# Optimization experiments

Measured on AMD Instinct MI355X. Metric: run time of the kernel, lower is better.

## Reference

```python
import jax, jax.numpy as jnp
import numpy as np

B, S, D_IN, D_OUT = 4, 2048, 1024, 1024


def setup_inputs() -> dict:
    key = jax.random.key(0)
    kx, kq, kk, kv = jax.random.split(key, 4)
    scale = 1.0 / np.sqrt(D_IN)
    return {
        "x": jax.random.normal(kx, (B, S, D_IN), dtype=jnp.float32),
        "W_q": jax.random.normal(kq, (D_IN, D_OUT), dtype=jnp.float32) * scale,
        "W_k": jax.random.normal(kk, (D_IN, D_OUT), dtype=jnp.float32) * scale,
        "W_v": jax.random.normal(kv, (D_IN, D_OUT), dtype=jnp.float32) * scale,
    }


def reference(x, W_q, W_k, W_v):
    # QKV projections (Linear without bias): [B,S,D_out]
    q = jnp.einsum("bsd,de->bse", x, W_q)
    k = jnp.einsum("bsd,de->bse", x, W_k)
    v = jnp.einsum("bsd,de->bse", x, W_v)

    # Raw scores [B,S,S], causal mask (strict upper triangle -> -inf),
    # then scale by sqrt(d_k) and softmax, matching the torch order of ops.
    scores = jnp.einsum("bqd,bkd->bqk", q, k)
    seq = scores.shape[-1]
    causal = jnp.triu(jnp.ones((seq, seq), dtype=bool), k=1)
    scores = jnp.where(causal[None, :, :], -jnp.inf, scores)
    attn = jax.nn.softmax(scores / jnp.sqrt(jnp.asarray(q.shape[-1], scores.dtype)), axis=-1)
    # dropout p=0.0 -> identity (eval semantics)
    return jnp.einsum("bqk,bkd->bqd", attn, v)
```

## Files before the change

### kernel.cpp

```cpp
#include <hip/hip_runtime.h>

typedef unsigned short u16;
typedef __bf16 bf16x8 __attribute__((ext_vector_type(8)));
typedef float f32x4 __attribute__((ext_vector_type(4)));

__device__ __forceinline__ u16 f2bf(float f) {
    union { float f; unsigned int u; } v; v.f = f;
    unsigned int u = v.u;
    return (u16)((u + 0x7FFFu + ((u >> 16) & 1u)) >> 16);
}

__device__ __forceinline__ void load_lds16(const void* g, void* l) {
    __builtin_amdgcn_global_load_lds(
        (const __attribute__((address_space(1))) unsigned int*)g,
        (__attribute__((address_space(3))) unsigned int*)l,
        16, 0, 0);
}

__global__ void __launch_bounds__(256) prep_kernel(
    const float4* __restrict__ X, u16* __restrict__ xb,
    const float* __restrict__ Wq, const float* __restrict__ Wk,
    const float* __restrict__ Wv,
    u16* __restrict__ Oq, u16* __restrict__ Ok, u16* __restrict__ Ov,
    float* __restrict__ rowsum) {
    __shared__ float tile[32][33];
    const int bid = blockIdx.x, tid = threadIdx.x;
    if (bid < 8192) {
        int idx = bid * 256 + tid;
        float4 v = X[idx];
        ushort4 o;
        o.x = f2bf(v.x); o.y = f2bf(v.y); o.z = f2bf(v.z); o.w = f2bf(v.w);
        *(ushort4*)(xb + (size_t)idx * 4) = o;
    } else if (bid < 11264) {
        int id = bid - 8192;
        int zz = id >> 10;
        const float* W = (zz == 0) ? Wq : (zz == 1) ? Wk : Wv;
        u16* O = (zz == 0) ? Oq : (zz == 1) ? Ok : Ov;
        int n0 = (id & 31) * 32, k0 = ((id >> 5) & 31) * 32;
        int tx = tid & 31, ty = tid >> 5;
        #pragma unroll
        for (int j = 0; j < 32; j += 8)
            tile[ty + j][tx] = W[(size_t)(k0 + ty + j) * 1024 + n0 + tx];
        __syncthreads();
        #pragma unroll
        for (int j = 0; j < 32; j += 8)
            O[(size_t)(n0 + ty + j) * 1024 + k0 + tx] = f2bf(tile[tx][ty + j]);
    } else {
        rowsum[(bid - 11264) * 256 + tid] = 0.f;
    }
}

template <int MODE>
__global__ void __launch_bounds__(256) gemm_nt(
    const u16* __restrict__ xb, const u16* __restrict__ WqT,
    const u16* __restrict__ WkT, const u16* __restrict__ WvT,
    u16* __restrict__ Q, u16* __restrict__ Kb,
    u16* __restrict__ Vt, u16* __restrict__ S,
    float* __restrict__ rowsum, float* __restrict__ out) {

    int mtile, ntile, z;
    const u16 *A, *B;
    int vsub = 0;

    if (MODE == 0) {
        int L = blockIdx.x;
        int c = L & 7, t = (L >> 3) & 7, hi = L >> 6;
        int p = hi * 8 + c;
        z = p >> 6; mtile = p & 63; ntile = t;
        A = xb;
        B = z ? WkT : WqT;
    } else if (MODE == 1) {
        if (blockIdx.x < 512) {
            vsub = 1;
            int id = blockIdx.x;
            int c = id & 7, t = (id >> 3) & 7, hi = id >> 6;
            mtile = hi * 8 + c; ntile = t; z = 0;
            A = xb; B = WvT;
        } else {
            int id2 = blockIdx.x - 512;
            z = id2 / 192;
            int r = id2 - z * 192;
            int c = r & 7, g = r >> 3;
            if (g <= c)            { mtile = c;     ntile = g; }
            else if (g < 2*c + 10) { mtile = c + 8; ntile = g - (c + 1); }
            else return;
            A = Q  + (size_t)z * (2048 * 1024);
            B = Kb + (size_t)z * (2048 * 1024);
        }
    } else {
        int L = blockIdx.x;
        ntile = L & 7;
        int j = L >> 3;
        z = j & 3; mtile = 15 - (j >> 2);
        A = S  + (size_t)z * (2048 * 2048);
        B = Vt + (size_t)z * (1024 * 2048);
    }

    const int LDA = (MODE == 3) ? 2048 : 1024;
    const int kiters = (MODE == 3) ? (mtile + 1) * 2 : 16;

    __shared__ __align__(16) u16 As[2][128 * 32];
    __shared__ __align__(16) u16 Bs[2][128 * 32];

    const int tid = threadIdx.x;
    const int lane = tid & 63;
    const int wave = tid >> 6;
    const int wr = wave >> 1, wc = wave & 1;

    const int r0 = tid >> 2;
    const int kb = (((tid & 3) ^ ((r0 >> 1) & 3))) * 16;

    const char* gA0 = (const char*)(A + (size_t)(mtile * 128 + r0) * LDA) + kb;
    const char* gA1 = gA0 + (size_t)64 * LDA * 2;
    const char* gB0 = (const char*)(B + (size_t)(ntile * 128 + r0) * LDA) + kb;
    const char* gB1 = gB0 + (size_t)64 * LDA * 2;

    char* lA = (char*)(&As[0][0]) + tid * 16;
    char* lB = (char*)(&Bs[0][0]) + tid * 16;

    f32x4 acc[4][4] = {};

    const int quad = lane >> 4;
    const int l16 = lane & 15;
    const int ch = quad ^ ((l16 >> 1) & 3);
    const int aoff = (wr * 64 + l16) * 32 + ch * 8;
    const int boff = (wc * 64 + l16) * 32 + ch * 8;

    for (int kt = 0; kt < kiters; ++kt) {
        load_lds16(gA0,      lA);
        load_lds16(gA1,      lA + 4096);
        load_lds16(gA0 + 64, lA + 8192);
        load_lds16(gA1 + 64, lA + 12288);
        load_lds16(gB0,      lB);
        load_lds16(gB1,      lB + 4096);
        load_lds16(gB0 + 64, lB + 8192);
        load_lds16(gB1 + 64, lB + 12288);
        gA0 += 128; gA1 += 128; gB0 += 128; gB1 += 128;
        __syncthreads();

        #pragma unroll
        for (int h2 = 0; h2 < 2; ++h2) {
            const u16* ap = &As[h2][aoff];
            const u16* bp = &Bs[h2][boff];
            bf16x8 af[4], bfv[4];
            #pragma unroll
            for (int r = 0; r < 4; ++r) af[r] = *(const bf16x8*)(ap + r * 512);
            #pragma unroll
            for (int c = 0; c < 4; ++c) bfv[c] = *(const bf16x8*)(bp + c * 512);
            #pragma unroll
            for (int r = 0; r < 4; ++r)
                #pragma unroll
                for (int c = 0; c < 4; ++c)
                    acc[r][c] = __builtin_amdgcn_mfma_f32_16x16x32_bf16(
                        af[r], bfv[c], acc[r][c], 0, 0, 0);
        }
        __syncthreads();
    }

    const int grow0 = mtile * 128 + wr * 64 + quad * 4;
    const int gcol0 = ntile * 128 + wc * 64 + l16;

    if (MODE == 0) {
        u16* C = z ? Kb : Q;
        #pragma unroll
        for (int r = 0; r < 4; ++r)
            #pragma unroll
            for (int c = 0; c < 4; ++c)
                #pragma unroll
                for (int i = 0; i < 4; ++i)
                    C[(size_t)(grow0 + r * 16 + i) * 1024 + gcol0 + c * 16] =
                        f2bf(acc[r][c][i]);
    } else if (MODE == 1) {
        if (vsub) {
            #pragma unroll
            for (int r = 0; r < 4; ++r) {
                int m0 = grow0 + r * 16;
                int b = m0 >> 11, s0 = m0 & 2047;
                #pragma unroll
                for (int c = 0; c < 4; ++c) {
                    int d = gcol0 + c * 16;
                    ushort4 o;
                    o.x = f2bf(acc[r][c][0]); o.y = f2bf(acc[r][c][1]);
                    o.z = f2bf(acc[r][c][2]); o.w = f2bf(acc[r][c][3]);
                    *(ushort4*)(Vt + (size_t)b * (1024 * 2048) + (size_t)d * 2048 + s0) = o;
                }
            }
        } else {
            u16* C = S + (size_t)z * (2048 * 2048);
            float* rs = rowsum + z * 2048;
            const bool diag = (ntile == mtile);
            float rsum[4][4];
            #pragma unroll
            for (int r = 0; r < 4; ++r)
                #pragma unroll
                for (int i = 0; i < 4; ++i) rsum[r][i] = 0.f;
            #pragma unroll
            for (int r = 0; r < 4; ++r)
                #pragma unroll
                for (int c = 0; c < 4; ++c)
                    #pragma unroll
                    for (int i = 0; i < 4; ++i) {
                        int grow = grow0 + r * 16 + i;
                        int gcol = gcol0 + c * 16;
                        float e = 0.f;
                        if (!diag || gcol <= grow)
                            e = __expf(acc[r][c][i] * 0.03125f - 12.0f);
                        C[(size_t)grow * 2048 + gcol] = f2bf(e);
                        rsum[r][i] += e;
                    }
            #pragma unroll
            for (int r = 0; r < 4; ++r)
                #pragma unroll
                for (int i = 0; i < 4; ++i) {
                    float s = rsum[r][i];
                    s += __shfl_xor(s, 1, 64);
                    s += __shfl_xor(s, 2, 64);
                    s += __shfl_xor(s, 4, 64);
                    s += __shfl_xor(s, 8, 64);
                    if (l16 == 0)
                        atomicAdd(&rs[grow0 + r * 16 + i], s);
                }
        }
    } else {
        const float* rs = rowsum + z * 2048;
        float* C = out + (size_t)z * (2048 * 1024);
        #pragma unroll
        for (int r = 0; r < 4; ++r)
            #pragma unroll
            for (int i = 0; i < 4; ++i) {
                int grow = grow0 + r * 16 + i;
                float inv = 1.0f / rs[grow];
                #pragma unroll
                for (int c = 0; c < 4; ++c)
                    C[(size_t)grow * 1024 + gcol0 + c * 16] = acc[r][c][i] * inv;
            }
    }
}

extern "C" void kernel_launch(void* const* d_in, const int* in_sizes, int n_in,
                              void* d_out, int out_size, void* d_ws, size_t ws_size,
                              hipStream_t stream) {
    const float* x  = (const float*)d_in[0];
    const float* Wq = (const float*)d_in[1];
    const float* Wk = (const float*)d_in[2];
    const float* Wv = (const float*)d_in[3];
    float* out = (float*)d_out;
    char* ws = (char*)d_ws;
    const size_t Mi = 1u << 20;

    u16* xb  = (u16*)(ws);
    u16* WqT = (u16*)(ws + 16 * Mi);
    u16* WkT = (u16*)(ws + 18 * Mi);
    u16* WvT = (u16*)(ws + 20 * Mi);
    u16* Q   = (u16*)(ws + 22 * Mi);
    u16* Kb  = (u16*)(ws + 38 * Mi);
    u16* Vt  = (u16*)(ws + 54 * Mi);
    u16* S   = (u16*)(ws + 70 * Mi);
    float* rowsum = (float*)(ws + 102 * Mi);

    prep_kernel<<<11296, 256, 0, stream>>>(
        (const float4*)x, xb, Wq, Wk, Wv, WqT, WkT, WvT, rowsum);

    gemm_nt<0><<<1024, 256, 0, stream>>>(xb, WqT, WkT, WvT, Q, Kb, Vt, S, rowsum, out);

    gemm_nt<1><<<1280, 256, 0, stream>>>(xb, WqT, WkT, WvT, Q, Kb, Vt, S, rowsum, out);

    gemm_nt<3><<<512, 256, 0, stream>>>(xb, WqT, WkT, WvT, Q, Kb, Vt, S, rowsum, out);
}
```

Before: 236.3 us.

## Double-buffer LDS loads in GEMM and move V projection into QK launch

The GEMM main loop now uses the two LDS halves as ping-pong buffers with a 32-wide K step. The next tile's global-to-LDS loads are issued before computing on the current one, so memory latency overlaps MFMA work. The V projection moves from the scores launch into the Q/K projection launch (1536 blocks), leaving the scores launch with only the causal QK^T tiles. The mode index for the PV GEMM changes from 3 to 2. Each iteration does half the MFMA work per barrier pair, so synchronisation overhead per FLOP rises.

```diff
diff --git a/kernel.cpp b/kernel.cpp
--- a/kernel.cpp
+++ b/kernel.cpp
@@ -60,7 +60,6 @@
 
     int mtile, ntile, z;
     const u16 *A, *B;
-    int vsub = 0;
 
     if (MODE == 0) {
         int L = blockIdx.x;
@@ -68,25 +67,17 @@
         int p = hi * 8 + c;
         z = p >> 6; mtile = p & 63; ntile = t;
         A = xb;
-        B = z ? WkT : WqT;
+        B = (z == 0) ? WqT : (z == 1) ? WkT : WvT;
     } else if (MODE == 1) {
-        if (blockIdx.x < 512) {
-            vsub = 1;
-            int id = blockIdx.x;
-            int c = id & 7, t = (id >> 3) & 7, hi = id >> 6;
-            mtile = hi * 8 + c; ntile = t; z = 0;
-            A = xb; B = WvT;
-        } else {
-            int id2 = blockIdx.x - 512;
-            z = id2 / 192;
-            int r = id2 - z * 192;
-            int c = r & 7, g = r >> 3;
-            if (g <= c)            { mtile = c;     ntile = g; }
-            else if (g < 2*c + 10) { mtile = c + 8; ntile = g - (c + 1); }
-            else return;
-            A = Q  + (size_t)z * (2048 * 1024);
-            B = Kb + (size_t)z * (2048 * 1024);
-        }
+        int id2 = blockIdx.x;
+        z = id2 / 192;
+        int r = id2 - z * 192;
+        int c = r & 7, g = r >> 3;
+        if (g <= c)            { mtile = c;     ntile = g; }
+        else if (g < 2*c + 10) { mtile = c + 8; ntile = g - (c + 1); }
+        else return;
+        A = Q  + (size_t)z * (2048 * 1024);
+        B = Kb + (size_t)z * (2048 * 1024);
     } else {
         int L = blockIdx.x;
         ntile = L & 7;
@@ -96,8 +87,8 @@
         B = Vt + (size_t)z * (1024 * 2048);
     }
 
-    const int LDA = (MODE == 3) ? 2048 : 1024;
-    const int kiters = (MODE == 3) ? (mtile + 1) * 2 : 16;
+    const int LDA = (MODE == 2) ? 2048 : 1024;
+    const int kiters = (MODE == 2) ? (mtile + 1) * 4 : 32;
 
     __shared__ __align__(16) u16 As[2][128 * 32];
     __shared__ __align__(16) u16 Bs[2][128 * 32];
@@ -126,52 +117,58 @@
     const int aoff = (wr * 64 + l16) * 32 + ch * 8;
     const int boff = (wc * 64 + l16) * 32 + ch * 8;
 
-    for (int kt = 0; kt < kiters; ++kt) {
-        load_lds16(gA0,      lA);
-        load_lds16(gA1,      lA + 4096);
-        load_lds16(gA0 + 64, lA + 8192);
-        load_lds16(gA1 + 64, lA + 12288);
-        load_lds16(gB0,      lB);
-        load_lds16(gB1,      lB + 4096);
-        load_lds16(gB0 + 64, lB + 8192);
-        load_lds16(gB1 + 64, lB + 12288);
-        gA0 += 128; gA1 += 128; gB0 += 128; gB1 += 128;
+#define STAGE(b) do {                                   \
+        load_lds16(gA0, lA + (b) * 8192);               \
+        load_lds16(gA1, lA + (b) * 8192 + 4096);        \
+        load_lds16(gB0, lB + (b) * 8192);               \
+        load_lds16(gB1, lB + (b) * 8192 + 4096);        \
+        gA0 += 64; gA1 += 64; gB0 += 64; gB1 += 64;     \
+    } while (0)
+
+#define COMPUTE(b) do {                                                       \
+        const u16* ap = &As[b][aoff];                                         \
+        const u16* bp = &Bs[b][boff];                                         \
+        bf16x8 af[4], bfv[4];                                                 \
+        _Pragma("unroll")                                                     \
+        for (int r = 0; r < 4; ++r) af[r] = *(const bf16x8*)(ap + r * 512);   \
+        _Pragma("unroll")                                                     \
+        for (int c = 0; c < 4; ++c) bfv[c] = *(const bf16x8*)(bp + c * 512);  \
+        _Pragma("unroll")                                                     \
+        for (int r = 0; r < 4; ++r)                                           \
+            _Pragma("unroll")                                                 \
+            for (int c = 0; c < 4; ++c)                                       \
+                acc[r][c] = __builtin_amdgcn_mfma_f32_16x16x32_bf16(          \
+                    af[r], bfv[c], acc[r][c], 0, 0, 0);                       \
+    } while (0)
+
+    STAGE(0);
+    __syncthreads();
+    for (int kt = 0; kt < kiters; kt += 2) {
+        STAGE(1);
+        COMPUTE(0);
         __syncthreads();
-
-        #pragma unroll
-        for (int h2 = 0; h2 < 2; ++h2) {
-            const u16* ap = &As[h2][aoff];
-            const u16* bp = &Bs[h2][boff];
-            bf16x8 af[4], bfv[4];
-            #pragma unroll
-            for (int r = 0; r < 4; ++r) af[r] = *(const bf16x8*)(ap + r * 512);
-            #pragma unroll
-            for (int c = 0; c < 4; ++c) bfv[c] = *(const bf16x8*)(bp + c * 512);
-            #pragma unroll
-            for (int r = 0; r < 4; ++r)
-                #pragma unroll
-                for (int c = 0; c < 4; ++c)
-                    acc[r][c] = __builtin_amdgcn_mfma_f32_16x16x32_bf16(
-                        af[r], bfv[c], acc[r][c], 0, 0, 0);
-        }
+        if (kt + 2 < kiters) STAGE(0);
+        COMPUTE(1);
         __syncthreads();
     }
+#undef STAGE
+#undef COMPUTE
 
     const int grow0 = mtile * 128 + wr * 64 + quad * 4;
     const int gcol0 = ntile * 128 + wc * 64 + l16;
 
     if (MODE == 0) {
-        u16* C = z ? Kb : Q;
-        #pragma unroll
-        for (int r = 0; r < 4; ++r)
-            #pragma unroll
-            for (int c = 0; c < 4; ++c)
-                #pragma unroll
-                for (int i = 0; i < 4; ++i)
-                    C[(size_t)(grow0 + r * 16 + i) * 1024 + gcol0 + c * 16] =
-                        f2bf(acc[r][c][i]);
-    } else if (MODE == 1) {
-        if (vsub) {
+        if (z < 2) {
+            u16* C = z ? Kb : Q;
+            #pragma unroll
+            for (int r = 0; r < 4; ++r)
+                #pragma unroll
+                for (int c = 0; c < 4; ++c)
+                    #pragma unroll
+                    for (int i = 0; i < 4; ++i)
+                        C[(size_t)(grow0 + r * 16 + i) * 1024 + gcol0 + c * 16] =
+                            f2bf(acc[r][c][i]);
+        } else {
             #pragma unroll
             for (int r = 0; r < 4; ++r) {
                 int m0 = grow0 + r * 16;
@@ -185,42 +182,42 @@
                     *(ushort4*)(Vt + (size_t)b * (1024 * 2048) + (size_t)d * 2048 + s0) = o;
                 }
             }
-        } else {
-            u16* C = S + (size_t)z * (2048 * 2048);
-            float* rs = rowsum + z * 2048;
-            const bool diag = (ntile == mtile);
-            float rsum[4][4];
-            #pragma unroll
-            for (int r = 0; r < 4; ++r)
-                #pragma unroll
-                for (int i = 0; i < 4; ++i) rsum[r][i] = 0.f;
-            #pragma unroll
-            for (int r = 0; r < 4; ++r)
-                #pragma unroll
-                for (int c = 0; c < 4; ++c)
-                    #pragma unroll
-                    for (int i = 0; i < 4; ++i) {
-                        int grow = grow0 + r * 16 + i;
-                        int gcol = gcol0 + c * 16;
-                        float e = 0.f;
-                        if (!diag || gcol <= grow)
-                            e = __expf(acc[r][c][i] * 0.03125f - 12.0f);
-                        C[(size_t)grow * 2048 + gcol] = f2bf(e);
-                        rsum[r][i] += e;
-                    }
-            #pragma unroll
-            for (int r = 0; r < 4; ++r)
+        }
+    } else if (MODE == 1) {
+        u16* C = S + (size_t)z * (2048 * 2048);
+        float* rs = rowsum + z * 2048;
+        const bool diag = (ntile == mtile);
+        float rsum[4][4];
+        #pragma unroll
+        for (int r = 0; r < 4; ++r)
+            #pragma unroll
+            for (int i = 0; i < 4; ++i) rsum[r][i] = 0.f;
+        #pragma unroll
+        for (int r = 0; r < 4; ++r)
+            #pragma unroll
+            for (int c = 0; c < 4; ++c)
                 #pragma unroll
                 for (int i = 0; i < 4; ++i) {
-                    float s = rsum[r][i];
-                    s += __shfl_xor(s, 1, 64);
-                    s += __shfl_xor(s, 2, 64);
-                    s += __shfl_xor(s, 4, 64);
-                    s += __shfl_xor(s, 8, 64);
-                    if (l16 == 0)
-                        atomicAdd(&rs[grow0 + r * 16 + i], s);
+                    int grow = grow0 + r * 16 + i;
+                    int gcol = gcol0 + c * 16;
+                    float e = 0.f;
+                    if (!diag || gcol <= grow)
+                        e = __expf(acc[r][c][i] * 0.03125f - 12.0f);
+                    C[(size_t)grow * 2048 + gcol] = f2bf(e);
+                    rsum[r][i] += e;
                 }
-        }
+        #pragma unroll
+        for (int r = 0; r < 4; ++r)
+            #pragma unroll
+            for (int i = 0; i < 4; ++i) {
+                float s = rsum[r][i];
+                s += __shfl_xor(s, 1, 64);
+                s += __shfl_xor(s, 2, 64);
+                s += __shfl_xor(s, 4, 64);
+                s += __shfl_xor(s, 8, 64);
+                if (l16 == 0)
+                    atomicAdd(&rs[grow0 + r * 16 + i], s);
+            }
     } else {
         const float* rs = rowsum + z * 2048;
         float* C = out + (size_t)z * (2048 * 1024);
@@ -261,9 +258,9 @@
     prep_kernel<<<11296, 256, 0, stream>>>(
         (const float4*)x, xb, Wq, Wk, Wv, WqT, WkT, WvT, rowsum);
 
-    gemm_nt<0><<<1024, 256, 0, stream>>>(xb, WqT, WkT, WvT, Q, Kb, Vt, S, rowsum, out);
-
-    gemm_nt<1><<<1280, 256, 0, stream>>>(xb, WqT, WkT, WvT, Q, Kb, Vt, S, rowsum, out);
-
-    gemm_nt<3><<<512, 256, 0, stream>>>(xb, WqT, WkT, WvT, Q, Kb, Vt, S, rowsum, out);
-}
+    gemm_nt<0><<<1536, 256, 0, stream>>>(xb, WqT, WkT, WvT, Q, Kb, Vt, S, rowsum, out);
+
+    gemm_nt<1><<<768, 256, 0, stream>>>(xb, WqT, WkT, WvT, Q, Kb, Vt, S, rowsum, out);
+
+    gemm_nt<2><<<512, 256, 0, stream>>>(xb, WqT, WkT, WvT, Q, Kb, Vt, S, rowsum, out);
+}
```

After: 278.9 us. 18.1% more time.

## Use 512-thread blocks with 8 waves and move V projection into QK launch

Applied to the files above, without the earlier changes.

Doubles the GEMM block size to 8 waves (2x4 wave grid, 64x32 per wave), so each thread issues half as many global-to-LDS loads and holds half the accumulators. The V projection moves out of the score kernel and into the first projection launch, which now computes Q, K and V in one grid. This is meant to raise occupancy and parallelism per tile and to balance the launches. In exchange each wave does less MFMA work per LDS fragment load, and the B-fragment reuse per wave drops.

```diff
diff --git a/kernel.cpp b/kernel.cpp
--- a/kernel.cpp
+++ b/kernel.cpp
@@ -51,7 +51,7 @@
 }
 
 template <int MODE>
-__global__ void __launch_bounds__(256) gemm_nt(
+__global__ void __launch_bounds__(512) gemm_nt(
     const u16* __restrict__ xb, const u16* __restrict__ WqT,
     const u16* __restrict__ WkT, const u16* __restrict__ WvT,
     u16* __restrict__ Q, u16* __restrict__ Kb,
@@ -60,7 +60,6 @@
 
     int mtile, ntile, z;
     const u16 *A, *B;
-    int vsub = 0;
 
     if (MODE == 0) {
         int L = blockIdx.x;
@@ -68,25 +67,17 @@
         int p = hi * 8 + c;
         z = p >> 6; mtile = p & 63; ntile = t;
         A = xb;
-        B = z ? WkT : WqT;
+        B = (z == 0) ? WqT : (z == 1) ? WkT : WvT;
     } else if (MODE == 1) {
-        if (blockIdx.x < 512) {
-            vsub = 1;
-            int id = blockIdx.x;
-            int c = id & 7, t = (id >> 3) & 7, hi = id >> 6;
-            mtile = hi * 8 + c; ntile = t; z = 0;
-            A = xb; B = WvT;
-        } else {
-            int id2 = blockIdx.x - 512;
-            z = id2 / 192;
-            int r = id2 - z * 192;
-            int c = r & 7, g = r >> 3;
-            if (g <= c)            { mtile = c;     ntile = g; }
-            else if (g < 2*c + 10) { mtile = c + 8; ntile = g - (c + 1); }
-            else return;
-            A = Q  + (size_t)z * (2048 * 1024);
-            B = Kb + (size_t)z * (2048 * 1024);
-        }
+        int id2 = blockIdx.x;
+        z = id2 / 192;
+        int r = id2 - z * 192;
+        int c = r & 7, g = r >> 3;
+        if (g <= c)            { mtile = c;     ntile = g; }
+        else if (g < 2*c + 10) { mtile = c + 8; ntile = g - (c + 1); }
+        else return;
+        A = Q  + (size_t)z * (2048 * 1024);
+        B = Kb + (size_t)z * (2048 * 1024);
     } else {
         int L = blockIdx.x;
         ntile = L & 7;
@@ -96,61 +87,55 @@
         B = Vt + (size_t)z * (1024 * 2048);
     }
 
-    const int LDA = (MODE == 3) ? 2048 : 1024;
-    const int kiters = (MODE == 3) ? (mtile + 1) * 2 : 16;
-
-    __shared__ __align__(16) u16 As[2][128 * 32];
-    __shared__ __align__(16) u16 Bs[2][128 * 32];
+    const int LDA = (MODE == 2) ? 2048 : 1024;
+    const int kiters = (MODE == 2) ? (mtile + 1) * 2 : 16;
+
+    __shared__ __align__(16) u16 As[128 * 64];
+    __shared__ __align__(16) u16 Bs[128 * 64];
 
     const int tid = threadIdx.x;
     const int lane = tid & 63;
     const int wave = tid >> 6;
-    const int wr = wave >> 1, wc = wave & 1;
+    const int wr = wave >> 2, wc = wave & 3;
 
     const int r0 = tid >> 2;
     const int kb = (((tid & 3) ^ ((r0 >> 1) & 3))) * 16;
 
-    const char* gA0 = (const char*)(A + (size_t)(mtile * 128 + r0) * LDA) + kb;
-    const char* gA1 = gA0 + (size_t)64 * LDA * 2;
-    const char* gB0 = (const char*)(B + (size_t)(ntile * 128 + r0) * LDA) + kb;
-    const char* gB1 = gB0 + (size_t)64 * LDA * 2;
-
-    char* lA = (char*)(&As[0][0]) + tid * 16;
-    char* lB = (char*)(&Bs[0][0]) + tid * 16;
-
-    f32x4 acc[4][4] = {};
+    const char* gA = (const char*)(A + (size_t)(mtile * 128 + r0) * LDA) + kb;
+    const char* gB = (const char*)(B + (size_t)(ntile * 128 + r0) * LDA) + kb;
+
+    char* lA = (char*)As + tid * 16;
+    char* lB = (char*)Bs + tid * 16;
+
+    f32x4 acc[4][2] = {};
 
     const int quad = lane >> 4;
     const int l16 = lane & 15;
     const int ch = quad ^ ((l16 >> 1) & 3);
     const int aoff = (wr * 64 + l16) * 32 + ch * 8;
-    const int boff = (wc * 64 + l16) * 32 + ch * 8;
+    const int boff = (wc * 32 + l16) * 32 + ch * 8;
 
     for (int kt = 0; kt < kiters; ++kt) {
-        load_lds16(gA0,      lA);
-        load_lds16(gA1,      lA + 4096);
-        load_lds16(gA0 + 64, lA + 8192);
-        load_lds16(gA1 + 64, lA + 12288);
-        load_lds16(gB0,      lB);
-        load_lds16(gB1,      lB + 4096);
-        load_lds16(gB0 + 64, lB + 8192);
-        load_lds16(gB1 + 64, lB + 12288);
-        gA0 += 128; gA1 += 128; gB0 += 128; gB1 += 128;
+        load_lds16(gA,      lA);
+        load_lds16(gA + 64, lA + 8192);
+        load_lds16(gB,      lB);
+        load_lds16(gB + 64, lB + 8192);
+        gA += 128; gB += 128;
         __syncthreads();
 
         #pragma unroll
-        for (int h2 = 0; h2 < 2; ++h2) {
-            const u16* ap = &As[h2][aoff];
-            const u16* bp = &Bs[h2][boff];
-            bf16x8 af[4], bfv[4];
+        for (int h = 0; h < 2; ++h) {
+            const u16* ap = As + h * 4096 + aoff;
+            const u16* bp = Bs + h * 4096 + boff;
+            bf16x8 af[4], bfv[2];
             #pragma unroll
             for (int r = 0; r < 4; ++r) af[r] = *(const bf16x8*)(ap + r * 512);
             #pragma unroll
-            for (int c = 0; c < 4; ++c) bfv[c] = *(const bf16x8*)(bp + c * 512);
+            for (int c = 0; c < 2; ++c) bfv[c] = *(const bf16x8*)(bp + c * 512);
             #pragma unroll
             for (int r = 0; r < 4; ++r)
                 #pragma unroll
-                for (int c = 0; c < 4; ++c)
+                for (int c = 0; c < 2; ++c)
                     acc[r][c] = __builtin_amdgcn_mfma_f32_16x16x32_bf16(
                         af[r], bfv[c], acc[r][c], 0, 0, 0);
         }
@@ -158,26 +143,26 @@
     }
 
     const int grow0 = mtile * 128 + wr * 64 + quad * 4;
-    const int gcol0 = ntile * 128 + wc * 64 + l16;
+    const int gcol0 = ntile * 128 + wc * 32 + l16;
 
     if (MODE == 0) {
-        u16* C = z ? Kb : Q;
-        #pragma unroll
-        for (int r = 0; r < 4; ++r)
-            #pragma unroll
-            for (int c = 0; c < 4; ++c)
-                #pragma unroll
-                for (int i = 0; i < 4; ++i)
-                    C[(size_t)(grow0 + r * 16 + i) * 1024 + gcol0 + c * 16] =
-                        f2bf(acc[r][c][i]);
-    } else if (MODE == 1) {
-        if (vsub) {
+        if (z < 2) {
+            u16* C = z ? Kb : Q;
+            #pragma unroll
+            for (int r = 0; r < 4; ++r)
+                #pragma unroll
+                for (int c = 0; c < 2; ++c)
+                    #pragma unroll
+                    for (int i = 0; i < 4; ++i)
+                        C[(size_t)(grow0 + r * 16 + i) * 1024 + gcol0 + c * 16] =
+                            f2bf(acc[r][c][i]);
+        } else {
             #pragma unroll
             for (int r = 0; r < 4; ++r) {
                 int m0 = grow0 + r * 16;
                 int b = m0 >> 11, s0 = m0 & 2047;
                 #pragma unroll
-                for (int c = 0; c < 4; ++c) {
+                for (int c = 0; c < 2; ++c) {
                     int d = gcol0 + c * 16;
                     ushort4 o;
                     o.x = f2bf(acc[r][c][0]); o.y = f2bf(acc[r][c][1]);
@@ -185,42 +170,42 @@
                     *(ushort4*)(Vt + (size_t)b * (1024 * 2048) + (size_t)d * 2048 + s0) = o;
                 }
             }
-        } else {
-            u16* C = S + (size_t)z * (2048 * 2048);
-            float* rs = rowsum + z * 2048;
-            const bool diag = (ntile == mtile);
-            float rsum[4][4];
-            #pragma unroll
-            for (int r = 0; r < 4; ++r)
-                #pragma unroll
-                for (int i = 0; i < 4; ++i) rsum[r][i] = 0.f;
-            #pragma unroll
-            for (int r = 0; r < 4; ++r)
-                #pragma unroll
-                for (int c = 0; c < 4; ++c)
-                    #pragma unroll
-                    for (int i = 0; i < 4; ++i) {
-                        int grow = grow0 + r * 16 + i;
-                        int gcol = gcol0 + c * 16;
-                        float e = 0.f;
-                        if (!diag || gcol <= grow)
-                            e = __expf(acc[r][c][i] * 0.03125f - 12.0f);
-                        C[(size_t)grow * 2048 + gcol] = f2bf(e);
-                        rsum[r][i] += e;
-                    }
-            #pragma unroll
-            for (int r = 0; r < 4; ++r)
+        }
+    } else if (MODE == 1) {
+        u16* C = S + (size_t)z * (2048 * 2048);
+        float* rs = rowsum + z * 2048;
+        const bool diag = (ntile == mtile);
+        float rsum[4][4];
+        #pragma unroll
+        for (int r = 0; r < 4; ++r)
+            #pragma unroll
+            for (int i = 0; i < 4; ++i) rsum[r][i] = 0.f;
+        #pragma unroll
+        for (int r = 0; r < 4; ++r)
+            #pragma unroll
+            for (int c = 0; c < 2; ++c)
                 #pragma unroll
                 for (int i = 0; i < 4; ++i) {
-                    float s = rsum[r][i];
-                    s += __shfl_xor(s, 1, 64);
-                    s += __shfl_xor(s, 2, 64);
-                    s += __shfl_xor(s, 4, 64);
-                    s += __shfl_xor(s, 8, 64);
-                    if (l16 == 0)
-                        atomicAdd(&rs[grow0 + r * 16 + i], s);
+                    int grow = grow0 + r * 16 + i;
+                    int gcol = gcol0 + c * 16;
+                    float e = 0.f;
+                    if (!diag || gcol <= grow)
+                        e = __expf(acc[r][c][i] * 0.03125f - 12.0f);
+                    C[(size_t)grow * 2048 + gcol] = f2bf(e);
+                    rsum[r][i] += e;
                 }
-        }
+        #pragma unroll
+        for (int r = 0; r < 4; ++r)
+            #pragma unroll
+            for (int i = 0; i < 4; ++i) {
+                float s = rsum[r][i];
+                s += __shfl_xor(s, 1, 64);
+                s += __shfl_xor(s, 2, 64);
+                s += __shfl_xor(s, 4, 64);
+                s += __shfl_xor(s, 8, 64);
+                if (l16 == 0)
+                    atomicAdd(&rs[grow0 + r * 16 + i], s);
+            }
     } else {
         const float* rs = rowsum + z * 2048;
         float* C = out + (size_t)z * (2048 * 1024);
@@ -231,7 +216,7 @@
                 int grow = grow0 + r * 16 + i;
                 float inv = 1.0f / rs[grow];
                 #pragma unroll
-                for (int c = 0; c < 4; ++c)
+                for (int c = 0; c < 2; ++c)
                     C[(size_t)grow * 1024 + gcol0 + c * 16] = acc[r][c][i] * inv;
             }
     }
@@ -261,9 +246,9 @@
     prep_kernel<<<11296, 256, 0, stream>>>(
         (const float4*)x, xb, Wq, Wk, Wv, WqT, WkT, WvT, rowsum);
 
-    gemm_nt<0><<<1024, 256, 0, stream>>>(xb, WqT, WkT, WvT, Q, Kb, Vt, S, rowsum, out);
-
-    gemm_nt<1><<<1280, 256, 0, stream>>>(xb, WqT, WkT, WvT, Q, Kb, Vt, S, rowsum, out);
-
-    gemm_nt<3><<<512, 256, 0, stream>>>(xb, WqT, WkT, WvT, Q, Kb, Vt, S, rowsum, out);
-}
+    gemm_nt<0><<<1536, 512, 0, stream>>>(xb, WqT, WkT, WvT, Q, Kb, Vt, S, rowsum, out);
+
+    gemm_nt<1><<<768, 512, 0, stream>>>(xb, WqT, WkT, WvT, Q, Kb, Vt, S, rowsum, out);
+
+    gemm_nt<2><<<512, 512, 0, stream>>>(xb, WqT, WkT, WvT, Q, Kb, Vt, S, rowsum, out);
+}
```

After: 222.5 us. 5.8% less time.
